# Kernel optimization log

Hardware: AMD Instinct MI355X
Metric: run time of the kernel (lower is better)

## Reference

```python
import jax, jax.numpy as jnp
import numpy as np

N_SYS = 64      # number of systems
N_ELEC = 64     # electrons per system
DIM = 256
HEADS = 8
EPS = 1e-6      # flax LayerNorm default epsilon


def _edge_indices():
    # all intra-system electron pairs (including self), block-diagonal structure
    ii, jj = np.meshgrid(np.arange(N_ELEC), np.arange(N_ELEC), indexing='ij')
    offs = (np.arange(N_SYS) * N_ELEC)[:, None, None]
    ei = (offs + ii[None]).reshape(-1).astype(np.int32)
    ej = (offs + jj[None]).reshape(-1).astype(np.int32)
    return jnp.asarray(ei), jnp.asarray(ej)


def setup_inputs() -> dict:
    key = jax.random.key(0)
    ks = jax.random.split(key, 8)
    n = N_SYS * N_ELEC
    ei, ej = _edge_indices()
    s = 1.0 / np.sqrt(DIM)
    return {
        'h_one': jax.random.normal(ks[0], (n, DIM), jnp.float32),
        'W_qkv': jax.random.normal(ks[1], (DIM, 3 * DIM), jnp.float32) * s,
        'W_out': jax.random.normal(ks[2], (DIM, DIM), jnp.float32) * s,
        'ln1_scale': jnp.ones((DIM,), jnp.float32),
        'ln1_bias': jnp.zeros((DIM,), jnp.float32),
        'W_mlp': jax.random.normal(ks[3], (DIM, DIM), jnp.float32) * s,
        'b_mlp': jnp.zeros((DIM,), jnp.float32),
        'ln2_scale': jnp.ones((DIM,), jnp.float32),
        'ln2_bias': jnp.zeros((DIM,), jnp.float32),
        'e_e_i': ei,
        'e_e_j': ej,
    }


def _layernorm(x, scale, bias):
    mu = jnp.mean(x, axis=-1, keepdims=True)
    var = jnp.mean(jnp.square(x - mu), axis=-1, keepdims=True)
    return (x - mu) * jax.lax.rsqrt(var + EPS) * scale + bias


def _segment_softmax(logits, seg, n):
    mx = jax.ops.segment_max(logits, seg, num_segments=n)
    e = jnp.exp(logits - mx[seg])
    denom = jax.ops.segment_sum(e, seg, num_segments=n)
    return e / denom[seg]


def reference(h_one, W_qkv, W_out, ln1_scale, ln1_bias, W_mlp, b_mlp,
              ln2_scale, ln2_bias, e_e_i, e_e_j):
    n = h_one.shape[0]
    hd = DIM // HEADS
    qkv = h_one @ W_qkv                                  # [n, 3*dim]
    Q, K, V = jnp.split(qkv, 3, axis=-1)
    Q = Q.reshape(n, HEADS, hd)
    K = K.reshape(n, HEADS, hd)
    V = V.reshape(n, HEADS, hd)
    # per-edge attention scores: Q[i] . K[j] over head dim -> [E, H]
    A = jnp.einsum('ehd,ehd->eh', Q[e_e_i], K[e_e_j]) / jnp.sqrt(jnp.float32(hd))
    # NOTE: softmax segmented by e_e_j, scatter-sum by e_e_i (faithful to source)
    A = _segment_softmax(A, e_e_j, n)
    attn = jax.ops.segment_sum(A[..., None] * V[e_e_j], e_e_i, num_segments=n)
    attn = attn.reshape(n, DIM)
    h = h_one + attn @ W_out
    h = _layernorm(h, ln1_scale, ln1_bias)
    h = h + jax.nn.silu(h @ W_mlp + b_mlp)
    h = _layernorm(h, ln2_scale, ln2_bias)
    return h
```

## Files before the change

### kernel.cpp

```cpp
#include <hip/hip_runtime.h>
#include <hip/hip_bf16.h>
#include <math.h>

#define N_SYS   64
#define N_ELEC  64
#define NTOT    (N_SYS * N_ELEC)
#define DIM     256
#define HEADS   8
#define LN_EPS  1e-6f

typedef __attribute__((ext_vector_type(8))) short bf16x8;
typedef __attribute__((ext_vector_type(4))) short short4v;
typedef __attribute__((ext_vector_type(4))) float f32x4;

static __device__ __forceinline__ short f2bf(float f) {
    __hip_bfloat16 h = __float2bfloat16(f);
    return *reinterpret_cast<short*>(&h);
}

__global__ __launch_bounds__(256) void k1_qkv_attn(
    const float* __restrict__ h_one, const float* __restrict__ W_qkv,
    const float* __restrict__ Wout, const float* __restrict__ Wmlp,
    short* __restrict__ attn, short* __restrict__ WoutT,
    short* __restrict__ WmlpT)
{
    const int tid = threadIdx.x;

    if (blockIdx.x >= 512) {
        const int b2 = blockIdx.x - 512;
        const float* src = (b2 < 16) ? Wout : Wmlp;
        short* dst = (b2 < 16) ? WoutT : WmlpT;
        const int tile = b2 & 15;
        const int tk = (tile >> 2) * 64, tn = (tile & 3) * 64;
#pragma unroll
        for (int p = 0; p < 4; ++p) {
            int idx = p * 256 + tid;
            int kk = idx >> 4, n4 = (idx & 15) * 4;
            float4 v = *(const float4*)&src[(size_t)(tk + kk) * 256 + tn + n4];
            dst[(size_t)(tn + n4 + 0) * 256 + tk + kk] = f2bf(v.x);
            dst[(size_t)(tn + n4 + 1) * 256 + tk + kk] = f2bf(v.y);
            dst[(size_t)(tn + n4 + 2) * 256 + tk + kk] = f2bf(v.z);
            dst[(size_t)(tn + n4 + 3) * 256 + tk + kk] = f2bf(v.w);
        }
        return;
    }

    const int s = blockIdx.x & 63;
    const int h = blockIdx.x >> 6;

    __shared__ short Ha[64][72];
    __shared__ short Bs[96][72];
    __shared__ short Qs[64][40];
    __shared__ short Ks[64][40];
    __shared__ short Vt[32][72];
    __shared__ short Pm[64][72];

    const int lane = tid & 63;
    const int w = tid >> 6;
    const int l15 = lane & 15;
    const int l4 = lane >> 4;

    const float* Abase = h_one + (size_t)s * 64 * 256;
    const int bkk = tid >> 2;
    const int btt = tid & 3;

    f32x4 acc[6] = {};

    for (int k0 = 0; k0 < 256; k0 += 64) {
        if (k0) __syncthreads();
#pragma unroll
        for (int it = 0; it < 2; ++it) {
            int c = it * 256 + tid;
            int r = c >> 3, c8 = (c & 7) * 8;
            const float* srcp = &Abase[(size_t)r * 256 + k0 + c8];
            float4 v0 = *(const float4*)srcp;
            float4 v1 = *(const float4*)(srcp + 4);
            bf16x8 o;
            o[0] = f2bf(v0.x); o[1] = f2bf(v0.y); o[2] = f2bf(v0.z); o[3] = f2bf(v0.w);
            o[4] = f2bf(v1.x); o[5] = f2bf(v1.y); o[6] = f2bf(v1.z); o[7] = f2bf(v1.w);
            *(bf16x8*)&Ha[r][c8] = o;
        }
#pragma unroll
        for (int q = 0; q < 6; ++q) {
            int c = btt + q * 4;
            int g = c >> 3;
            int c4 = (c & 7) * 4;
            float4 v = *(const float4*)&W_qkv[(size_t)(k0 + bkk) * 768 + g * 256 + h * 32 + c4];
            Bs[g * 32 + c4 + 0][bkk] = f2bf(v.x);
            Bs[g * 32 + c4 + 1][bkk] = f2bf(v.y);
            Bs[g * 32 + c4 + 2][bkk] = f2bf(v.z);
            Bs[g * 32 + c4 + 3][bkk] = f2bf(v.w);
        }
        __syncthreads();
#pragma unroll
        for (int ki = 0; ki < 2; ++ki) {
            bf16x8 af = *(const bf16x8*)&Ha[w * 16 + l15][ki * 32 + l4 * 8];
#pragma unroll
            for (int nf = 0; nf < 6; ++nf) {
                bf16x8 bfv = *(const bf16x8*)&Bs[nf * 16 + l15][ki * 32 + l4 * 8];
                acc[nf] = __builtin_amdgcn_mfma_f32_16x16x32_bf16(af, bfv, acc[nf], 0, 0, 0);
            }
        }
    }

#pragma unroll
    for (int nf = 0; nf < 6; ++nf) {
        int c = nf * 16 + l15;
#pragma unroll
        for (int j = 0; j < 4; ++j) {
            int row = w * 16 + l4 * 4 + j;
            short v = f2bf(acc[nf][j]);
            if (c < 32)       Qs[row][c] = v;
            else if (c < 64)  Ks[row][c - 32] = v;
            else              Vt[c - 64][row] = v;
        }
    }
    __syncthreads();

    const float scale = 0.17677669529663687f;
    f32x4 sacc[4] = {};
    {
        bf16x8 ak = *(const bf16x8*)&Ks[w * 16 + l15][l4 * 8];
#pragma unroll
        for (int nf = 0; nf < 4; ++nf) {
            bf16x8 bq = *(const bf16x8*)&Qs[nf * 16 + l15][l4 * 8];
            sacc[nf] = __builtin_amdgcn_mfma_f32_16x16x32_bf16(ak, bq, sacc[nf], 0, 0, 0);
        }
    }
#pragma unroll
    for (int nf = 0; nf < 4; ++nf) sacc[nf] *= scale;
#pragma unroll
    for (int jj = 0; jj < 4; ++jj) {
        float mx = fmaxf(fmaxf(sacc[0][jj], sacc[1][jj]),
                         fmaxf(sacc[2][jj], sacc[3][jj]));
        mx = fmaxf(mx, __shfl_xor(mx, 1, 64));
        mx = fmaxf(mx, __shfl_xor(mx, 2, 64));
        mx = fmaxf(mx, __shfl_xor(mx, 4, 64));
        mx = fmaxf(mx, __shfl_xor(mx, 8, 64));
        float e0 = __expf(sacc[0][jj] - mx);
        float e1 = __expf(sacc[1][jj] - mx);
        float e2 = __expf(sacc[2][jj] - mx);
        float e3 = __expf(sacc[3][jj] - mx);
        float ss = e0 + e1 + e2 + e3;
        ss += __shfl_xor(ss, 1, 64);
        ss += __shfl_xor(ss, 2, 64);
        ss += __shfl_xor(ss, 4, 64);
        ss += __shfl_xor(ss, 8, 64);
        float inv = 1.0f / ss;
        sacc[0][jj] = e0 * inv; sacc[1][jj] = e1 * inv;
        sacc[2][jj] = e2 * inv; sacc[3][jj] = e3 * inv;
    }
#pragma unroll
    for (int nf = 0; nf < 4; ++nf) {
        short4v pq;
        pq[0] = f2bf(sacc[nf][0]); pq[1] = f2bf(sacc[nf][1]);
        pq[2] = f2bf(sacc[nf][2]); pq[3] = f2bf(sacc[nf][3]);
        *(short4v*)&Pm[nf * 16 + l15][w * 16 + l4 * 4] = pq;
    }
    __syncthreads();

    f32x4 pv[2] = {};
#pragma unroll
    for (int ki = 0; ki < 2; ++ki) {
        bf16x8 ap = *(const bf16x8*)&Pm[w * 16 + l15][ki * 32 + l4 * 8];
#pragma unroll
        for (int nf = 0; nf < 2; ++nf) {
            bf16x8 bv = *(const bf16x8*)&Vt[nf * 16 + l15][ki * 32 + l4 * 8];
            pv[nf] = __builtin_amdgcn_mfma_f32_16x16x32_bf16(ap, bv, pv[nf], 0, 0, 0);
        }
    }
#pragma unroll
    for (int nf = 0; nf < 2; ++nf)
#pragma unroll
        for (int j = 0; j < 4; ++j)
            attn[(size_t)(s * 64 + w * 16 + l4 * 4 + j) * 256 + h * 32 + nf * 16 + l15]
                = f2bf(pv[nf][j]);
}

__global__ __launch_bounds__(512) void k2_tail(
    const short* __restrict__ attnbf, const short* __restrict__ WoutT,
    const short* __restrict__ WmlpT, const float* __restrict__ h_one,
    const float* __restrict__ b_mlp,
    const float* __restrict__ ln1_s, const float* __restrict__ ln1_b,
    const float* __restrict__ ln2_s, const float* __restrict__ ln2_b,
    float* __restrict__ out)
{
    const int r0 = blockIdx.x * 16;

    __shared__ short Abf[16][264];
    __shared__ float H1[16][260];
    __shared__ short L1[16][264];

    const int tid = threadIdx.x;
    const int lane = tid & 63;
    const int w = tid >> 6;
    const int l15 = lane & 15;
    const int l4 = lane >> 4;

    {
        int r = tid >> 5, c8 = (tid & 31) * 8;
        *(bf16x8*)&Abf[r][c8] = *(const bf16x8*)&attnbf[(size_t)(r0 + r) * 256 + c8];
    }
    __syncthreads();

    f32x4 acc[2] = {};
    for (int k0 = 0; k0 < 256; k0 += 32) {
        bf16x8 af = *(const bf16x8*)&Abf[l15][k0 + l4 * 8];
#pragma unroll
        for (int nf = 0; nf < 2; ++nf) {
            int n = w * 32 + nf * 16 + l15;
            bf16x8 bf = *(const bf16x8*)&WoutT[(size_t)n * 256 + k0 + l4 * 8];
            acc[nf] = __builtin_amdgcn_mfma_f32_16x16x32_bf16(af, bf, acc[nf], 0, 0, 0);
        }
    }
#pragma unroll
    for (int nf = 0; nf < 2; ++nf) {
        int col = w * 32 + nf * 16 + l15;
#pragma unroll
        for (int j = 0; j < 4; ++j) {
            int row = l4 * 4 + j;
            H1[row][col] = acc[nf][j] + h_one[(size_t)(r0 + row) * 256 + col];
        }
    }
    __syncthreads();

    {
        float4 sc = *(const float4*)&ln1_s[lane * 4];
        float4 bi = *(const float4*)&ln1_b[lane * 4];
#pragma unroll
        for (int rr = 0; rr < 2; ++rr) {
            int row = w * 2 + rr;
            float4 v = *(const float4*)&H1[row][lane * 4];
            float su = v.x + v.y + v.z + v.w;
#pragma unroll
            for (int off = 32; off > 0; off >>= 1) su += __shfl_xor(su, off, 64);
            float mu = su * (1.0f / 256.0f);
            float dx = v.x - mu, dy = v.y - mu, dz = v.z - mu, dw = v.w - mu;
            float s2 = dx * dx + dy * dy + dz * dz + dw * dw;
#pragma unroll
            for (int off = 32; off > 0; off >>= 1) s2 += __shfl_xor(s2, off, 64);
            float inv = rsqrtf(s2 * (1.0f / 256.0f) + LN_EPS);
            float4 o;
            o.x = dx * inv * sc.x + bi.x;
            o.y = dy * inv * sc.y + bi.y;
            o.z = dz * inv * sc.z + bi.z;
            o.w = dw * inv * sc.w + bi.w;
            *(float4*)&H1[row][lane * 4] = o;
            short4v ob;
            ob[0] = f2bf(o.x); ob[1] = f2bf(o.y); ob[2] = f2bf(o.z); ob[3] = f2bf(o.w);
            *(short4v*)&L1[row][lane * 4] = ob;
        }
    }
    __syncthreads();

    f32x4 acc2[2] = {};
    for (int k0 = 0; k0 < 256; k0 += 32) {
        bf16x8 af = *(const bf16x8*)&L1[l15][k0 + l4 * 8];
#pragma unroll
        for (int nf = 0; nf < 2; ++nf) {
            int n = w * 32 + nf * 16 + l15;
            bf16x8 bf = *(const bf16x8*)&WmlpT[(size_t)n * 256 + k0 + l4 * 8];
            acc2[nf] = __builtin_amdgcn_mfma_f32_16x16x32_bf16(af, bf, acc2[nf], 0, 0, 0);
        }
    }
#pragma unroll
    for (int nf = 0; nf < 2; ++nf) {
        int col = w * 32 + nf * 16 + l15;
        float bm = b_mlp[col];
#pragma unroll
        for (int j = 0; j < 4; ++j) {
            int row = l4 * 4 + j;
            float v = acc2[nf][j] + bm;
            float sg = 1.0f / (1.0f + __expf(-v));
            H1[row][col] = H1[row][col] + v * sg;
        }
    }
    __syncthreads();

    {
        float4 sc = *(const float4*)&ln2_s[lane * 4];
        float4 bi = *(const float4*)&ln2_b[lane * 4];
#pragma unroll
        for (int rr = 0; rr < 2; ++rr) {
            int row = w * 2 + rr;
            float4 v = *(const float4*)&H1[row][lane * 4];
            float su = v.x + v.y + v.z + v.w;
#pragma unroll
            for (int off = 32; off > 0; off >>= 1) su += __shfl_xor(su, off, 64);
            float mu = su * (1.0f / 256.0f);
            float dx = v.x - mu, dy = v.y - mu, dz = v.z - mu, dw = v.w - mu;
            float s2 = dx * dx + dy * dy + dz * dz + dw * dw;
#pragma unroll
            for (int off = 32; off > 0; off >>= 1) s2 += __shfl_xor(s2, off, 64);
            float inv = rsqrtf(s2 * (1.0f / 256.0f) + LN_EPS);
            float4 o;
            o.x = dx * inv * sc.x + bi.x;
            o.y = dy * inv * sc.y + bi.y;
            o.z = dz * inv * sc.z + bi.z;
            o.w = dw * inv * sc.w + bi.w;
            *(float4*)&out[(size_t)(r0 + row) * 256 + lane * 4] = o;
        }
    }
}

extern "C" void kernel_launch(void* const* d_in, const int* in_sizes, int n_in,
                              void* d_out, int out_size, void* d_ws, size_t ws_size,
                              hipStream_t stream)
{
    const float* h_one = (const float*)d_in[0];
    const float* W_qkv = (const float*)d_in[1];
    const float* W_out = (const float*)d_in[2];
    const float* ln1_s = (const float*)d_in[3];
    const float* ln1_b = (const float*)d_in[4];
    const float* W_mlp = (const float*)d_in[5];
    const float* b_mlp = (const float*)d_in[6];
    const float* ln2_s = (const float*)d_in[7];
    const float* ln2_b = (const float*)d_in[8];
    float* out = (float*)d_out;

    char* ws = (char*)d_ws;
    short* attn_bf = (short*)ws;
    short* WoutT   = (short*)(ws + 2097152);
    short* WmlpT   = WoutT + 256 * 256;

    k1_qkv_attn<<<544, 256, 0, stream>>>(h_one, W_qkv, W_out, W_mlp,
                                         attn_bf, WoutT, WmlpT);
    k2_tail<<<256, 512, 0, stream>>>(attn_bf, WoutT, WmlpT, h_one, b_mlp,
                                     ln1_s, ln1_b, ln2_s, ln2_b, out);
}
```

Before: 26.20 us.

## Process two systems per block in QKV-attention kernel, sharing staged weight tile

Each block of the first kernel now handles two systems for one head, using 512 threads, so the converted W_qkv tile in shared memory is reused across twice as many rows. The h_one activation is no longer staged through LDS; each wave loads its A fragment directly from global memory and converts it to bf16 in registers. The weight-transpose blocks are packed two tiles per block, halving the grid. This cuts redundant weight loads and LDS traffic but halves block count, which lowers parallelism, and the direct A loads from global memory are less coalesced.

```diff
diff --git a/kernel.cpp b/kernel.cpp
--- a/kernel.cpp
+++ b/kernel.cpp
@@ -18,7 +18,7 @@
     return *reinterpret_cast<short*>(&h);
 }
 
-__global__ __launch_bounds__(256) void k1_qkv_attn(
+__global__ __launch_bounds__(512, 4) void k1_qkv_attn(
     const float* __restrict__ h_one, const float* __restrict__ W_qkv,
     const float* __restrict__ Wout, const float* __restrict__ Wmlp,
     short* __restrict__ attn, short* __restrict__ WoutT,
@@ -26,15 +26,16 @@
 {
     const int tid = threadIdx.x;
 
-    if (blockIdx.x >= 512) {
-        const int b2 = blockIdx.x - 512;
-        const float* src = (b2 < 16) ? Wout : Wmlp;
-        short* dst = (b2 < 16) ? WoutT : WmlpT;
-        const int tile = b2 & 15;
+    if (blockIdx.x >= 256) {
+        const int t2 = (blockIdx.x - 256) * 2 + (tid >> 8);
+        const int ltid = tid & 255;
+        const float* src = (t2 < 16) ? Wout : Wmlp;
+        short* dst = (t2 < 16) ? WoutT : WmlpT;
+        const int tile = t2 & 15;
         const int tk = (tile >> 2) * 64, tn = (tile & 3) * 64;
 #pragma unroll
         for (int p = 0; p < 4; ++p) {
-            int idx = p * 256 + tid;
+            int idx = p * 256 + ltid;
             int kk = idx >> 4, n4 = (idx & 15) * 4;
             float4 v = *(const float4*)&src[(size_t)(tk + kk) * 256 + tn + n4];
             dst[(size_t)(tn + n4 + 0) * 256 + tk + kk] = f2bf(v.x);
@@ -45,44 +46,36 @@
         return;
     }
 
-    const int s = blockIdx.x & 63;
-    const int h = blockIdx.x >> 6;
-
-    __shared__ short Ha[64][72];
+    const int h = blockIdx.x >> 5;
+    const int p = blockIdx.x & 31;
+
     __shared__ short Bs[96][72];
-    __shared__ short Qs[64][40];
-    __shared__ short Ks[64][40];
-    __shared__ short Vt[32][72];
-    __shared__ short Pm[64][72];
+    __shared__ short Qs[2][64][40];
+    __shared__ short Ks[2][64][40];
+    __shared__ short Vt[2][32][72];
+    __shared__ short Pm[2][64][72];
 
     const int lane = tid & 63;
     const int w = tid >> 6;
+    const int sysw = w >> 2;
+    const int wl = w & 3;
     const int l15 = lane & 15;
     const int l4 = lane >> 4;
 
-    const float* Abase = h_one + (size_t)s * 64 * 256;
-    const int bkk = tid >> 2;
-    const int btt = tid & 3;
+    const int s = p * 2 + sysw;
+
+    const float* Arow = h_one + ((size_t)s * 64 + wl * 16 + l15) * 256;
+
+    const int bkk = tid >> 3;
+    const int btt = tid & 7;
 
     f32x4 acc[6] = {};
 
     for (int k0 = 0; k0 < 256; k0 += 64) {
         if (k0) __syncthreads();
 #pragma unroll
-        for (int it = 0; it < 2; ++it) {
-            int c = it * 256 + tid;
-            int r = c >> 3, c8 = (c & 7) * 8;
-            const float* srcp = &Abase[(size_t)r * 256 + k0 + c8];
-            float4 v0 = *(const float4*)srcp;
-            float4 v1 = *(const float4*)(srcp + 4);
-            bf16x8 o;
-            o[0] = f2bf(v0.x); o[1] = f2bf(v0.y); o[2] = f2bf(v0.z); o[3] = f2bf(v0.w);
-            o[4] = f2bf(v1.x); o[5] = f2bf(v1.y); o[6] = f2bf(v1.z); o[7] = f2bf(v1.w);
-            *(bf16x8*)&Ha[r][c8] = o;
-        }
-#pragma unroll
-        for (int q = 0; q < 6; ++q) {
-            int c = btt + q * 4;
+        for (int q = 0; q < 3; ++q) {
+            int c = btt + q * 8;
             int g = c >> 3;
             int c4 = (c & 7) * 4;
             float4 v = *(const float4*)&W_qkv[(size_t)(k0 + bkk) * 768 + g * 256 + h * 32 + c4];
@@ -94,7 +87,12 @@
         __syncthreads();
 #pragma unroll
         for (int ki = 0; ki < 2; ++ki) {
-            bf16x8 af = *(const bf16x8*)&Ha[w * 16 + l15][ki * 32 + l4 * 8];
+            const float* ap = Arow + k0 + ki * 32 + l4 * 8;
+            float4 a0 = *(const float4*)ap;
+            float4 a1 = *(const float4*)(ap + 4);
+            bf16x8 af;
+            af[0] = f2bf(a0.x); af[1] = f2bf(a0.y); af[2] = f2bf(a0.z); af[3] = f2bf(a0.w);
+            af[4] = f2bf(a1.x); af[5] = f2bf(a1.y); af[6] = f2bf(a1.z); af[7] = f2bf(a1.w);
 #pragma unroll
             for (int nf = 0; nf < 6; ++nf) {
                 bf16x8 bfv = *(const bf16x8*)&Bs[nf * 16 + l15][ki * 32 + l4 * 8];
@@ -108,11 +106,11 @@
         int c = nf * 16 + l15;
 #pragma unroll
         for (int j = 0; j < 4; ++j) {
-            int row = w * 16 + l4 * 4 + j;
+            int row = wl * 16 + l4 * 4 + j;
             short v = f2bf(acc[nf][j]);
-            if (c < 32)       Qs[row][c] = v;
-            else if (c < 64)  Ks[row][c - 32] = v;
-            else              Vt[c - 64][row] = v;
+            if (c < 32)       Qs[sysw][row][c] = v;
+            else if (c < 64)  Ks[sysw][row][c - 32] = v;
+            else              Vt[sysw][c - 64][row] = v;
         }
     }
     __syncthreads();
@@ -120,10 +118,10 @@
     const float scale = 0.17677669529663687f;
     f32x4 sacc[4] = {};
     {
-        bf16x8 ak = *(const bf16x8*)&Ks[w * 16 + l15][l4 * 8];
+        bf16x8 ak = *(const bf16x8*)&Ks[sysw][wl * 16 + l15][l4 * 8];
 #pragma unroll
         for (int nf = 0; nf < 4; ++nf) {
-            bf16x8 bq = *(const bf16x8*)&Qs[nf * 16 + l15][l4 * 8];
+            bf16x8 bq = *(const bf16x8*)&Qs[sysw][nf * 16 + l15][l4 * 8];
             sacc[nf] = __builtin_amdgcn_mfma_f32_16x16x32_bf16(ak, bq, sacc[nf], 0, 0, 0);
         }
     }
@@ -155,17 +153,17 @@
         short4v pq;
         pq[0] = f2bf(sacc[nf][0]); pq[1] = f2bf(sacc[nf][1]);
         pq[2] = f2bf(sacc[nf][2]); pq[3] = f2bf(sacc[nf][3]);
-        *(short4v*)&Pm[nf * 16 + l15][w * 16 + l4 * 4] = pq;
+        *(short4v*)&Pm[sysw][nf * 16 + l15][wl * 16 + l4 * 4] = pq;
     }
     __syncthreads();
 
     f32x4 pv[2] = {};
 #pragma unroll
     for (int ki = 0; ki < 2; ++ki) {
-        bf16x8 ap = *(const bf16x8*)&Pm[w * 16 + l15][ki * 32 + l4 * 8];
+        bf16x8 ap = *(const bf16x8*)&Pm[sysw][wl * 16 + l15][ki * 32 + l4 * 8];
 #pragma unroll
         for (int nf = 0; nf < 2; ++nf) {
-            bf16x8 bv = *(const bf16x8*)&Vt[nf * 16 + l15][ki * 32 + l4 * 8];
+            bf16x8 bv = *(const bf16x8*)&Vt[sysw][nf * 16 + l15][ki * 32 + l4 * 8];
             pv[nf] = __builtin_amdgcn_mfma_f32_16x16x32_bf16(ap, bv, pv[nf], 0, 0, 0);
         }
     }
@@ -173,7 +171,7 @@
     for (int nf = 0; nf < 2; ++nf)
 #pragma unroll
         for (int j = 0; j < 4; ++j)
-            attn[(size_t)(s * 64 + w * 16 + l4 * 4 + j) * 256 + h * 32 + nf * 16 + l15]
+            attn[(size_t)(s * 64 + wl * 16 + l4 * 4 + j) * 256 + h * 32 + nf * 16 + l15]
                 = f2bf(pv[nf][j]);
 }
 
@@ -323,7 +321,7 @@
     short* WoutT   = (short*)(ws + 2097152);
     short* WmlpT   = WoutT + 256 * 256;
 
-    k1_qkv_attn<<<544, 256, 0, stream>>>(h_one, W_qkv, W_out, W_mlp,
+    k1_qkv_attn<<<272, 512, 0, stream>>>(h_one, W_qkv, W_out, W_mlp,
                                          attn_bf, WoutT, WmlpT);
     k2_tail<<<256, 512, 0, stream>>>(attn_bf, WoutT, WmlpT, h_one, b_mlp,
                                      ln1_s, ln1_b, ln2_s, ln2_b, out);
```

Result: slower. 28.74 us (+9.7%).

## Fuse attention and tail kernels into one launch with atomic-counter dependencies

Applied to the files above, without the earlier changes.

Merges the QKV/attention kernel and the output-projection/MLP/LayerNorm tail kernel into a single launch. The first 256 attention blocks go on to do the tail work, spin-waiting on per-system and weight-transpose atomic counters. It also adds register double-buffering of the global loads in the QKV GEMM loop and uses a shared-memory union so both phases fit in one block. The tail phase now runs with 256 threads per block instead of 512. This removes one kernel launch boundary but adds a memset, spin-wait latency, and a deadlock risk if the producer blocks are not resident.

```diff
diff --git a/kernel.cpp b/kernel.cpp
--- a/kernel.cpp
+++ b/kernel.cpp
@@ -18,16 +18,42 @@
     return *reinterpret_cast<short*>(&h);
 }
 
-__global__ __launch_bounds__(256) void k1_qkv_attn(
+__global__ __launch_bounds__(256, 3) void fused_k(
     const float* __restrict__ h_one, const float* __restrict__ W_qkv,
     const float* __restrict__ Wout, const float* __restrict__ Wmlp,
+    const float* __restrict__ b_mlp,
+    const float* __restrict__ ln1_s, const float* __restrict__ ln1_b,
+    const float* __restrict__ ln2_s, const float* __restrict__ ln2_b,
+    float* __restrict__ out,
     short* __restrict__ attn, short* __restrict__ WoutT,
-    short* __restrict__ WmlpT)
+    short* __restrict__ WmlpT, unsigned* __restrict__ cnt)
 {
     const int tid = threadIdx.x;
-
-    if (blockIdx.x >= 512) {
-        const int b2 = blockIdx.x - 512;
+    const int bid = blockIdx.x;
+
+    __shared__ union {
+        struct {
+            short Ha[64][72];
+            short Bs[96][72];
+            short Qs[64][40];
+            short Ks[64][40];
+            short Vt[32][72];
+            short Pm[64][72];
+        } p1;
+        struct {
+            short Abf[16][264];
+            float H1[16][260];
+            short L1[16][264];
+        } p2;
+    } sm;
+
+    const int lane = tid & 63;
+    const int w = tid >> 6;
+    const int l15 = lane & 15;
+    const int l4 = lane >> 4;
+
+    if (bid < 32) {
+        const int b2 = bid;
         const float* src = (b2 < 16) ? Wout : Wmlp;
         short* dst = (b2 < 16) ? WoutT : WmlpT;
         const int tile = b2 & 15;
@@ -42,184 +68,210 @@
             dst[(size_t)(tn + n4 + 2) * 256 + tk + kk] = f2bf(v.z);
             dst[(size_t)(tn + n4 + 3) * 256 + tk + kk] = f2bf(v.w);
         }
+        __syncthreads();
+        if (tid == 0) { __threadfence(); atomicAdd(&cnt[64], 1u); }
         return;
     }
 
-    const int s = blockIdx.x & 63;
-    const int h = blockIdx.x >> 6;
-
-    __shared__ short Ha[64][72];
-    __shared__ short Bs[96][72];
-    __shared__ short Qs[64][40];
-    __shared__ short Ks[64][40];
-    __shared__ short Vt[32][72];
-    __shared__ short Pm[64][72];
-
-    const int lane = tid & 63;
-    const int w = tid >> 6;
-    const int l15 = lane & 15;
-    const int l4 = lane >> 4;
-
-    const float* Abase = h_one + (size_t)s * 64 * 256;
-    const int bkk = tid >> 2;
-    const int btt = tid & 3;
-
-    f32x4 acc[6] = {};
-
-    for (int k0 = 0; k0 < 256; k0 += 64) {
-        if (k0) __syncthreads();
-#pragma unroll
-        for (int it = 0; it < 2; ++it) {
-            int c = it * 256 + tid;
-            int r = c >> 3, c8 = (c & 7) * 8;
-            const float* srcp = &Abase[(size_t)r * 256 + k0 + c8];
-            float4 v0 = *(const float4*)srcp;
-            float4 v1 = *(const float4*)(srcp + 4);
-            bf16x8 o;
-            o[0] = f2bf(v0.x); o[1] = f2bf(v0.y); o[2] = f2bf(v0.z); o[3] = f2bf(v0.w);
-            o[4] = f2bf(v1.x); o[5] = f2bf(v1.y); o[6] = f2bf(v1.z); o[7] = f2bf(v1.w);
-            *(bf16x8*)&Ha[r][c8] = o;
-        }
-#pragma unroll
-        for (int q = 0; q < 6; ++q) {
-            int c = btt + q * 4;
-            int g = c >> 3;
-            int c4 = (c & 7) * 4;
-            float4 v = *(const float4*)&W_qkv[(size_t)(k0 + bkk) * 768 + g * 256 + h * 32 + c4];
-            Bs[g * 32 + c4 + 0][bkk] = f2bf(v.x);
-            Bs[g * 32 + c4 + 1][bkk] = f2bf(v.y);
-            Bs[g * 32 + c4 + 2][bkk] = f2bf(v.z);
-            Bs[g * 32 + c4 + 3][bkk] = f2bf(v.w);
+    const int pb = bid - 32;
+    const int s = pb & 63;
+    const int h = pb >> 6;
+
+    {
+        auto& P = sm.p1;
+        const float* Abase = h_one + (size_t)s * 64 * 256;
+        const int rA = tid >> 3;
+        const int cA8 = (tid & 7) * 8;
+        const int bkk = tid >> 2;
+        const int btt = tid & 3;
+
+        float4 ra[2][4];
+        float4 rb[2][6];
+
+#define K1_LOAD(buf, kbase)                                                        \
+        do {                                                                       \
+            const float* ap0 = &Abase[(size_t)rA * 256 + (kbase) + cA8];           \
+            const float* ap1 = &Abase[(size_t)(rA + 32) * 256 + (kbase) + cA8];    \
+            ra[buf][0] = *(const float4*)ap0;                                      \
+            ra[buf][1] = *(const float4*)(ap0 + 4);                                \
+            ra[buf][2] = *(const float4*)ap1;                                      \
+            ra[buf][3] = *(const float4*)(ap1 + 4);                                \
+            _Pragma("unroll")                                                      \
+            for (int q = 0; q < 6; ++q) {                                          \
+                int c = btt + q * 4;                                               \
+                int g = c >> 3;                                                    \
+                int c4 = (c & 7) * 4;                                              \
+                rb[buf][q] = *(const float4*)&W_qkv[(size_t)((kbase) + bkk) * 768  \
+                                                    + g * 256 + h * 32 + c4];      \
+            }                                                                      \
+        } while (0)
+
+        f32x4 acc[6] = {};
+        K1_LOAD(0, 0);
+
+#pragma unroll
+        for (int kk = 0; kk < 4; ++kk) {
+            const int k0 = kk * 64;
+            const int cur = kk & 1;
+            const int nxt = cur ^ 1;
+
+            if (kk) __syncthreads();
+            {
+                bf16x8 o;
+                o[0] = f2bf(ra[cur][0].x); o[1] = f2bf(ra[cur][0].y);
+                o[2] = f2bf(ra[cur][0].z); o[3] = f2bf(ra[cur][0].w);
+                o[4] = f2bf(ra[cur][1].x); o[5] = f2bf(ra[cur][1].y);
+                o[6] = f2bf(ra[cur][1].z); o[7] = f2bf(ra[cur][1].w);
+                *(bf16x8*)&P.Ha[rA][cA8] = o;
+                o[0] = f2bf(ra[cur][2].x); o[1] = f2bf(ra[cur][2].y);
+                o[2] = f2bf(ra[cur][2].z); o[3] = f2bf(ra[cur][2].w);
+                o[4] = f2bf(ra[cur][3].x); o[5] = f2bf(ra[cur][3].y);
+                o[6] = f2bf(ra[cur][3].z); o[7] = f2bf(ra[cur][3].w);
+                *(bf16x8*)&P.Ha[rA + 32][cA8] = o;
+            }
+#pragma unroll
+            for (int q = 0; q < 6; ++q) {
+                int c = btt + q * 4;
+                int g = c >> 3;
+                int c4 = (c & 7) * 4;
+                P.Bs[g * 32 + c4 + 0][bkk] = f2bf(rb[cur][q].x);
+                P.Bs[g * 32 + c4 + 1][bkk] = f2bf(rb[cur][q].y);
+                P.Bs[g * 32 + c4 + 2][bkk] = f2bf(rb[cur][q].z);
+                P.Bs[g * 32 + c4 + 3][bkk] = f2bf(rb[cur][q].w);
+            }
+            if (kk < 3) K1_LOAD(nxt, k0 + 64);
+            __syncthreads();
+
+#pragma unroll
+            for (int ki = 0; ki < 2; ++ki) {
+                bf16x8 af = *(const bf16x8*)&P.Ha[w * 16 + l15][ki * 32 + l4 * 8];
+#pragma unroll
+                for (int nf = 0; nf < 6; ++nf) {
+                    bf16x8 bfv = *(const bf16x8*)&P.Bs[nf * 16 + l15][ki * 32 + l4 * 8];
+                    acc[nf] = __builtin_amdgcn_mfma_f32_16x16x32_bf16(af, bfv, acc[nf], 0, 0, 0);
+                }
+            }
+        }
+#undef K1_LOAD
+
+#pragma unroll
+        for (int nf = 0; nf < 6; ++nf) {
+            int c = nf * 16 + l15;
+#pragma unroll
+            for (int j = 0; j < 4; ++j) {
+                int row = w * 16 + l4 * 4 + j;
+                short v = f2bf(acc[nf][j]);
+                if (c < 32)       P.Qs[row][c] = v;
+                else if (c < 64)  P.Ks[row][c - 32] = v;
+                else              P.Vt[c - 64][row] = v;
+            }
         }
         __syncthreads();
+
+        const float scale = 0.17677669529663687f;
+        f32x4 sacc[4] = {};
+        {
+            bf16x8 ak = *(const bf16x8*)&P.Ks[w * 16 + l15][l4 * 8];
+#pragma unroll
+            for (int nf = 0; nf < 4; ++nf) {
+                bf16x8 bq = *(const bf16x8*)&P.Qs[nf * 16 + l15][l4 * 8];
+                sacc[nf] = __builtin_amdgcn_mfma_f32_16x16x32_bf16(ak, bq, sacc[nf], 0, 0, 0);
+            }
+        }
+#pragma unroll
+        for (int nf = 0; nf < 4; ++nf) sacc[nf] *= scale;
+#pragma unroll
+        for (int jj = 0; jj < 4; ++jj) {
+            float mx = fmaxf(fmaxf(sacc[0][jj], sacc[1][jj]),
+                             fmaxf(sacc[2][jj], sacc[3][jj]));
+            mx = fmaxf(mx, __shfl_xor(mx, 1, 64));
+            mx = fmaxf(mx, __shfl_xor(mx, 2, 64));
+            mx = fmaxf(mx, __shfl_xor(mx, 4, 64));
+            mx = fmaxf(mx, __shfl_xor(mx, 8, 64));
+            float e0 = __expf(sacc[0][jj] - mx);
+            float e1 = __expf(sacc[1][jj] - mx);
+            float e2 = __expf(sacc[2][jj] - mx);
+            float e3 = __expf(sacc[3][jj] - mx);
+            float ss = e0 + e1 + e2 + e3;
+            ss += __shfl_xor(ss, 1, 64);
+            ss += __shfl_xor(ss, 2, 64);
+            ss += __shfl_xor(ss, 4, 64);
+            ss += __shfl_xor(ss, 8, 64);
+            float inv = 1.0f / ss;
+            sacc[0][jj] = e0 * inv; sacc[1][jj] = e1 * inv;
+            sacc[2][jj] = e2 * inv; sacc[3][jj] = e3 * inv;
+        }
+#pragma unroll
+        for (int nf = 0; nf < 4; ++nf) {
+            short4v pq;
+            pq[0] = f2bf(sacc[nf][0]); pq[1] = f2bf(sacc[nf][1]);
+            pq[2] = f2bf(sacc[nf][2]); pq[3] = f2bf(sacc[nf][3]);
+            *(short4v*)&P.Pm[nf * 16 + l15][w * 16 + l4 * 4] = pq;
+        }
+        __syncthreads();
+
+        f32x4 pv[2] = {};
 #pragma unroll
         for (int ki = 0; ki < 2; ++ki) {
-            bf16x8 af = *(const bf16x8*)&Ha[w * 16 + l15][ki * 32 + l4 * 8];
-#pragma unroll
-            for (int nf = 0; nf < 6; ++nf) {
-                bf16x8 bfv = *(const bf16x8*)&Bs[nf * 16 + l15][ki * 32 + l4 * 8];
-                acc[nf] = __builtin_amdgcn_mfma_f32_16x16x32_bf16(af, bfv, acc[nf], 0, 0, 0);
-            }
-        }
-    }
-
-#pragma unroll
-    for (int nf = 0; nf < 6; ++nf) {
-        int c = nf * 16 + l15;
-#pragma unroll
-        for (int j = 0; j < 4; ++j) {
-            int row = w * 16 + l4 * 4 + j;
-            short v = f2bf(acc[nf][j]);
-            if (c < 32)       Qs[row][c] = v;
-            else if (c < 64)  Ks[row][c - 32] = v;
-            else              Vt[c - 64][row] = v;
-        }
-    }
-    __syncthreads();
-
-    const float scale = 0.17677669529663687f;
-    f32x4 sacc[4] = {};
-    {
-        bf16x8 ak = *(const bf16x8*)&Ks[w * 16 + l15][l4 * 8];
+            bf16x8 ap = *(const bf16x8*)&P.Pm[w * 16 + l15][ki * 32 + l4 * 8];
+#pragma unroll
+            for (int nf = 0; nf < 2; ++nf) {
+                bf16x8 bv = *(const bf16x8*)&P.Vt[nf * 16 + l15][ki * 32 + l4 * 8];
+                pv[nf] = __builtin_amdgcn_mfma_f32_16x16x32_bf16(ap, bv, pv[nf], 0, 0, 0);
+            }
+        }
+#pragma unroll
+        for (int nf = 0; nf < 2; ++nf)
+#pragma unroll
+            for (int j = 0; j < 4; ++j)
+                attn[(size_t)(s * 64 + w * 16 + l4 * 4 + j) * 256 + h * 32 + nf * 16 + l15]
+                    = f2bf(pv[nf][j]);
+    }
+
+    __syncthreads();
+    if (tid == 0) { __threadfence(); atomicAdd(&cnt[s], 1u); }
+
+    if (pb >= 256) return;
+
+    const int s2 = (pb & 7) + ((pb >> 5) << 3);
+    const int rg = (pb >> 3) & 3;
+    const int r0 = s2 * 64 + rg * 16;
+
+    if (tid == 0) {
+        int guard = 0;
+        while (atomicAdd(&cnt[64], 0u) < 32u && guard < (1 << 22)) { __builtin_amdgcn_s_sleep(2); ++guard; }
+        guard = 0;
+        while (atomicAdd(&cnt[s2], 0u) < 8u && guard < (1 << 22)) { __builtin_amdgcn_s_sleep(2); ++guard; }
+    }
+    __syncthreads();
+
+    auto& T = sm.p2;
+
+#pragma unroll
+    for (int cc = 0; cc < 2; ++cc) {
+        int c = tid * 2 + cc;
+        int r = c >> 5, c8 = (c & 31) * 8;
+        *(bf16x8*)&T.Abf[r][c8] = *(const bf16x8*)&attn[(size_t)(r0 + r) * 256 + c8];
+    }
+    __syncthreads();
+
+    f32x4 acc[4] = {};
+    for (int k0 = 0; k0 < 256; k0 += 32) {
+        bf16x8 af = *(const bf16x8*)&T.Abf[l15][k0 + l4 * 8];
 #pragma unroll
         for (int nf = 0; nf < 4; ++nf) {
-            bf16x8 bq = *(const bf16x8*)&Qs[nf * 16 + l15][l4 * 8];
-            sacc[nf] = __builtin_amdgcn_mfma_f32_16x16x32_bf16(ak, bq, sacc[nf], 0, 0, 0);
-        }
-    }
-#pragma unroll
-    for (int nf = 0; nf < 4; ++nf) sacc[nf] *= scale;
-#pragma unroll
-    for (int jj = 0; jj < 4; ++jj) {
-        float mx = fmaxf(fmaxf(sacc[0][jj], sacc[1][jj]),
-                         fmaxf(sacc[2][jj], sacc[3][jj]));
-        mx = fmaxf(mx, __shfl_xor(mx, 1, 64));
-        mx = fmaxf(mx, __shfl_xor(mx, 2, 64));
-        mx = fmaxf(mx, __shfl_xor(mx, 4, 64));
-        mx = fmaxf(mx, __shfl_xor(mx, 8, 64));
-        float e0 = __expf(sacc[0][jj] - mx);
-        float e1 = __expf(sacc[1][jj] - mx);
-        float e2 = __expf(sacc[2][jj] - mx);
-        float e3 = __expf(sacc[3][jj] - mx);
-        float ss = e0 + e1 + e2 + e3;
-        ss += __shfl_xor(ss, 1, 64);
-        ss += __shfl_xor(ss, 2, 64);
-        ss += __shfl_xor(ss, 4, 64);
-        ss += __shfl_xor(ss, 8, 64);
-        float inv = 1.0f / ss;
-        sacc[0][jj] = e0 * inv; sacc[1][jj] = e1 * inv;
-        sacc[2][jj] = e2 * inv; sacc[3][jj] = e3 * inv;
-    }
-#pragma unroll
-    for (int nf = 0; nf < 4; ++nf) {
-        short4v pq;
-        pq[0] = f2bf(sacc[nf][0]); pq[1] = f2bf(sacc[nf][1]);
-        pq[2] = f2bf(sacc[nf][2]); pq[3] = f2bf(sacc[nf][3]);
-        *(short4v*)&Pm[nf * 16 + l15][w * 16 + l4 * 4] = pq;
-    }
-    __syncthreads();
-
-    f32x4 pv[2] = {};
-#pragma unroll
-    for (int ki = 0; ki < 2; ++ki) {
-        bf16x8 ap = *(const bf16x8*)&Pm[w * 16 + l15][ki * 32 + l4 * 8];
-#pragma unroll
-        for (int nf = 0; nf < 2; ++nf) {
-            bf16x8 bv = *(const bf16x8*)&Vt[nf * 16 + l15][ki * 32 + l4 * 8];
-            pv[nf] = __builtin_amdgcn_mfma_f32_16x16x32_bf16(ap, bv, pv[nf], 0, 0, 0);
-        }
-    }
-#pragma unroll
-    for (int nf = 0; nf < 2; ++nf)
-#pragma unroll
-        for (int j = 0; j < 4; ++j)
-            attn[(size_t)(s * 64 + w * 16 + l4 * 4 + j) * 256 + h * 32 + nf * 16 + l15]
-                = f2bf(pv[nf][j]);
-}
-
-__global__ __launch_bounds__(512) void k2_tail(
-    const short* __restrict__ attnbf, const short* __restrict__ WoutT,
-    const short* __restrict__ WmlpT, const float* __restrict__ h_one,
-    const float* __restrict__ b_mlp,
-    const float* __restrict__ ln1_s, const float* __restrict__ ln1_b,
-    const float* __restrict__ ln2_s, const float* __restrict__ ln2_b,
-    float* __restrict__ out)
-{
-    const int r0 = blockIdx.x * 16;
-
-    __shared__ short Abf[16][264];
-    __shared__ float H1[16][260];
-    __shared__ short L1[16][264];
-
-    const int tid = threadIdx.x;
-    const int lane = tid & 63;
-    const int w = tid >> 6;
-    const int l15 = lane & 15;
-    const int l4 = lane >> 4;
-
-    {
-        int r = tid >> 5, c8 = (tid & 31) * 8;
-        *(bf16x8*)&Abf[r][c8] = *(const bf16x8*)&attnbf[(size_t)(r0 + r) * 256 + c8];
-    }
-    __syncthreads();
-
-    f32x4 acc[2] = {};
-    for (int k0 = 0; k0 < 256; k0 += 32) {
-        bf16x8 af = *(const bf16x8*)&Abf[l15][k0 + l4 * 8];
-#pragma unroll
-        for (int nf = 0; nf < 2; ++nf) {
-            int n = w * 32 + nf * 16 + l15;
+            int n = w * 64 + nf * 16 + l15;
             bf16x8 bf = *(const bf16x8*)&WoutT[(size_t)n * 256 + k0 + l4 * 8];
             acc[nf] = __builtin_amdgcn_mfma_f32_16x16x32_bf16(af, bf, acc[nf], 0, 0, 0);
         }
     }
 #pragma unroll
-    for (int nf = 0; nf < 2; ++nf) {
-        int col = w * 32 + nf * 16 + l15;
+    for (int nf = 0; nf < 4; ++nf) {
+        int col = w * 64 + nf * 16 + l15;
 #pragma unroll
         for (int j = 0; j < 4; ++j) {
             int row = l4 * 4 + j;
-            H1[row][col] = acc[nf][j] + h_one[(size_t)(r0 + row) * 256 + col];
+            T.H1[row][col] = acc[nf][j] + h_one[(size_t)(r0 + row) * 256 + col];
         }
     }
     __syncthreads();
@@ -228,51 +280,51 @@
         float4 sc = *(const float4*)&ln1_s[lane * 4];
         float4 bi = *(const float4*)&ln1_b[lane * 4];
 #pragma unroll
-        for (int rr = 0; rr < 2; ++rr) {
-            int row = w * 2 + rr;
-            float4 v = *(const float4*)&H1[row][lane * 4];
+        for (int rr = 0; rr < 4; ++rr) {
+            int row = w * 4 + rr;
+            float4 v = *(const float4*)&T.H1[row][lane * 4];
             float su = v.x + v.y + v.z + v.w;
 #pragma unroll
             for (int off = 32; off > 0; off >>= 1) su += __shfl_xor(su, off, 64);
             float mu = su * (1.0f / 256.0f);
             float dx = v.x - mu, dy = v.y - mu, dz = v.z - mu, dw = v.w - mu;
-            float s2 = dx * dx + dy * dy + dz * dz + dw * dw;
-#pragma unroll
-            for (int off = 32; off > 0; off >>= 1) s2 += __shfl_xor(s2, off, 64);
-            float inv = rsqrtf(s2 * (1.0f / 256.0f) + LN_EPS);
+            float s2v = dx * dx + dy * dy + dz * dz + dw * dw;
+#pragma unroll
+            for (int off = 32; off > 0; off >>= 1) s2v += __shfl_xor(s2v, off, 64);
+            float inv = rsqrtf(s2v * (1.0f / 256.0f) + LN_EPS);
             float4 o;
             o.x = dx * inv * sc.x + bi.x;
             o.y = dy * inv * sc.y + bi.y;
             o.z = dz * inv * sc.z + bi.z;
             o.w = dw * inv * sc.w + bi.w;
-            *(float4*)&H1[row][lane * 4] = o;
+            *(float4*)&T.H1[row][lane * 4] = o;
             short4v ob;
             ob[0] = f2bf(o.x); ob[1] = f2bf(o.y); ob[2] = f2bf(o.z); ob[3] = f2bf(o.w);
-            *(short4v*)&L1[row][lane * 4] = ob;
-        }
-    }
-    __syncthreads();
-
-    f32x4 acc2[2] = {};
+            *(short4v*)&T.L1[row][lane * 4] = ob;
+        }
+    }
+    __syncthreads();
+
+    f32x4 acc2[4] = {};
     for (int k0 = 0; k0 < 256; k0 += 32) {
-        bf16x8 af = *(const bf16x8*)&L1[l15][k0 + l4 * 8];
-#pragma unroll
-        for (int nf = 0; nf < 2; ++nf) {
-            int n = w * 32 + nf * 16 + l15;
+        bf16x8 af = *(const bf16x8*)&T.L1[l15][k0 + l4 * 8];
+#pragma unroll
+        for (int nf = 0; nf < 4; ++nf) {
+            int n = w * 64 + nf * 16 + l15;
             bf16x8 bf = *(const bf16x8*)&WmlpT[(size_t)n * 256 + k0 + l4 * 8];
             acc2[nf] = __builtin_amdgcn_mfma_f32_16x16x32_bf16(af, bf, acc2[nf], 0, 0, 0);
         }
     }
 #pragma unroll
-    for (int nf = 0; nf < 2; ++nf) {
-        int col = w * 32 + nf * 16 + l15;
+    for (int nf = 0; nf < 4; ++nf) {
+        int col = w * 64 + nf * 16 + l15;
         float bm = b_mlp[col];
 #pragma unroll
         for (int j = 0; j < 4; ++j) {
             int row = l4 * 4 + j;
             float v = acc2[nf][j] + bm;
             float sg = 1.0f / (1.0f + __expf(-v));
-            H1[row][col] = H1[row][col] + v * sg;
+            T.H1[row][col] += v * sg;
         }
     }
     __syncthreads();
@@ -281,18 +333,18 @@
         float4 sc = *(const float4*)&ln2_s[lane * 4];
         float4 bi = *(const float4*)&ln2_b[lane * 4];
 #pragma unroll
-        for (int rr = 0; rr < 2; ++rr) {
-            int row = w * 2 + rr;
-            float4 v = *(const float4*)&H1[row][lane * 4];
+        for (int rr = 0; rr < 4; ++rr) {
+            int row = w * 4 + rr;
+            float4 v = *(const float4*)&T.H1[row][lane * 4];
             float su = v.x + v.y + v.z + v.w;
 #pragma unroll
             for (int off = 32; off > 0; off >>= 1) su += __shfl_xor(su, off, 64);
             float mu = su * (1.0f / 256.0f);
             float dx = v.x - mu, dy = v.y - mu, dz = v.z - mu, dw = v.w - mu;
-            float s2 = dx * dx + dy * dy + dz * dz + dw * dw;
-#pragma unroll
-            for (int off = 32; off > 0; off >>= 1) s2 += __shfl_xor(s2, off, 64);
-            float inv = rsqrtf(s2 * (1.0f / 256.0f) + LN_EPS);
+            float s2v = dx * dx + dy * dy + dz * dz + dw * dw;
+#pragma unroll
+            for (int off = 32; off > 0; off >>= 1) s2v += __shfl_xor(s2v, off, 64);
+            float inv = rsqrtf(s2v * (1.0f / 256.0f) + LN_EPS);
             float4 o;
             o.x = dx * inv * sc.x + bi.x;
             o.y = dy * inv * sc.y + bi.y;
@@ -322,9 +374,10 @@
     short* attn_bf = (short*)ws;
     short* WoutT   = (short*)(ws + 2097152);
     short* WmlpT   = WoutT + 256 * 256;
-
-    k1_qkv_attn<<<544, 256, 0, stream>>>(h_one, W_qkv, W_out, W_mlp,
-                                         attn_bf, WoutT, WmlpT);
-    k2_tail<<<256, 512, 0, stream>>>(attn_bf, WoutT, WmlpT, h_one, b_mlp,
-                                     ln1_s, ln1_b, ln2_s, ln2_b, out);
+    unsigned* cnt  = (unsigned*)(ws + 2097152 + 262144);
+
+    hipMemsetAsync(cnt, 0, 65 * sizeof(unsigned), stream);
+    fused_k<<<544, 256, 0, stream>>>(h_one, W_qkv, W_out, W_mlp, b_mlp,
+                                     ln1_s, ln1_b, ln2_s, ln2_b, out,
+                                     attn_bf, WoutT, WmlpT, cnt);
 }
```

After: 63.36 us. 2.42x slower.
